# Kernel tuning notes

Measured on AMD Instinct MI355X. Metric: run time of the kernel, lower is better.

## Reference

```python
import jax, jax.numpy as jnp
import numpy as np
import math

B, S, D, H, FF, L = 8, 1024, 1024, 8, 4096, 2
DK = D // H
NEG = -1e32
EPS = 1e-5


def _cosine_pe(seq_len, d_model):
    pos = jnp.arange(seq_len, dtype=jnp.float32)[:, None]
    div = jnp.exp(jnp.arange(0, d_model, 2, dtype=jnp.float32) * (-(math.log(10000.0) / d_model)))
    pe = jnp.zeros((seq_len, d_model), dtype=jnp.float32)
    pe = pe.at[:, 0::2].set(jnp.sin(pos * div))
    pe = pe.at[:, 1::2].set(jnp.cos(pos * div))
    return pe


def setup_inputs() -> dict:
    key = jax.random.key(0)
    ks = jax.random.split(key, 12)
    sc = 0.02
    g = lambda k, shape: (jax.random.normal(k, shape, jnp.float32) * sc)
    return {
        "q_embed": jax.random.normal(ks[0], (B, S, D), jnp.float32),
        "qa_embed": jax.random.normal(ks[1], (B, S, D), jnp.float32),
        "pos_emb": _cosine_pe(S, D),
        "Wk": g(ks[2], (L, D, D)), "bk": jnp.zeros((L, D), jnp.float32),
        "Wv": g(ks[3], (L, D, D)), "bv": jnp.zeros((L, D), jnp.float32),
        "Wo": g(ks[4], (L, D, D)), "bo": jnp.zeros((L, D), jnp.float32),
        "ln1_g": jnp.ones((L, D), jnp.float32), "ln1_b": jnp.zeros((L, D), jnp.float32),
        "W1": g(ks[5], (L, FF, D)), "b1": jnp.zeros((L, FF), jnp.float32),
        "W2": g(ks[6], (L, D, FF)), "b2": jnp.zeros((L, D), jnp.float32),
        "ln2_g": jnp.ones((L, D), jnp.float32), "ln2_b": jnp.zeros((L, D), jnp.float32),
    }


def _layernorm(x, g, b):
    m = jnp.mean(x, axis=-1, keepdims=True)
    v = jnp.mean(jnp.square(x - m), axis=-1, keepdims=True)
    return (x - m) * jax.lax.rsqrt(v + EPS) * g + b


def _mha(x, y, Wk, bk, Wv, bv, Wo, bo, allow):
    # kq_same=1: q and k both come from k_linear applied to x (query==key input)
    k = (jnp.einsum('bsd,od->bso', x, Wk) + bk).reshape(B, S, H, DK).transpose(0, 2, 1, 3)
    q = k  # identical projection and identical input
    v = (jnp.einsum('bsd,od->bso', y, Wv) + bv).reshape(B, S, H, DK).transpose(0, 2, 1, 3)
    scores = jnp.einsum('bhqd,bhkd->bhqk', q, k) / math.sqrt(DK)
    scores = jnp.where(allow, scores, NEG)  # masked_fill(mask==0, -1e32)
    attn = jax.nn.softmax(scores, axis=-1)
    attn = attn.at[:, :, 0, :].set(0.0)  # zero_pad: first query row zeroed
    out = jnp.einsum('bhqk,bhkd->bhqd', attn, v)
    out = out.transpose(0, 2, 1, 3).reshape(B, S, D)
    return jnp.einsum('bsd,od->bso', out, Wo) + bo


def reference(q_embed, qa_embed, pos_emb, Wk, bk, Wv, bv, Wo, bo,
              ln1_g, ln1_b, W1, b1, W2, b2, ln2_g, ln2_b):
    x = q_embed + pos_emb[None]
    y = qa_embed + pos_emb[None]
    # strictly-lower-triangular allowed positions (triu(k=0)==0)
    allow = jnp.tril(jnp.ones((S, S), dtype=bool), -1)[None, None]
    for l in range(L):
        q2 = _mha(x, x, y, Wk[l], bk[l], Wv[l], bv[l], Wo[l], bo[l], allow) if False else _mha(x, y, Wk[l], bk[l], Wv[l], bv[l], Wo[l], bo[l], allow)
        x = _layernorm(x + q2, ln1_g[l], ln1_b[l])
        ff = jnp.einsum('bsf,df->bsd', jax.nn.relu(jnp.einsum('bsd,fd->bsf', x, W1[l]) + b1[l]), W2[l]) + b2[l]
        x = _layernorm(x + ff, ln2_g[l], ln2_b[l])
    return x
```

## Files before the change

kernel.cpp:

```cpp
#include <hip/hip_runtime.h>
#include <hip/hip_bf16.h>
#include <cstdint>
#include <cstddef>

#define B_  8
#define S_  1024
#define D_  1024
#define H_  8
#define FF_ 4096
#define L_  2
#define DK_ 128

typedef __bf16 bf16x8 __attribute__((ext_vector_type(8)));
typedef float  f32x4  __attribute__((ext_vector_type(4)));

__device__ __forceinline__ unsigned short f2bf(float f) {
    union { float f; uint32_t u; } v; v.f = f;
    uint32_t r = v.u + 0x7fffu + ((v.u >> 16) & 1u);
    return (unsigned short)(r >> 16);
}
__device__ __forceinline__ float bf2f(unsigned short u) {
    union { uint32_t u; float f; } v; v.u = ((uint32_t)u) << 16; return v.f;
}

__global__ __launch_bounds__(256) void init_xy(
    const float* __restrict__ qe, const float* __restrict__ qa,
    const float* __restrict__ pe,
    unsigned short* __restrict__ xb, unsigned short* __restrict__ yb)
{
    int i = (blockIdx.x * 256 + threadIdx.x) * 4;
    int pi = i & (S_ * D_ - 1);
    float4 q = *(const float4*)(qe + i);
    float4 a = *(const float4*)(qa + i);
    float4 p = *(const float4*)(pe + pi);
    ushort4 xo; xo.x = f2bf(q.x + p.x); xo.y = f2bf(q.y + p.y);
    xo.z = f2bf(q.z + p.z); xo.w = f2bf(q.w + p.w);
    ushort4 yo; yo.x = f2bf(a.x + p.x); yo.y = f2bf(a.y + p.y);
    yo.z = f2bf(a.z + p.z); yo.w = f2bf(a.w + p.w);
    *(ushort4*)(xb + i) = xo;
    *(ushort4*)(yb + i) = yo;
}

__global__ __launch_bounds__(256) void cvt_bf16(
    const float* __restrict__ in, unsigned short* __restrict__ out)
{
    int i = (blockIdx.x * 256 + threadIdx.x) * 4;
    float4 f = *(const float4*)(in + i);
    ushort4 o; o.x = f2bf(f.x); o.y = f2bf(f.y); o.z = f2bf(f.z); o.w = f2bf(f.w);
    *(ushort4*)(out + i) = o;
}

template<bool RELU, int OMODE>
__global__ __launch_bounds__(256) void gemm_bt(
    const unsigned short* __restrict__ A, const unsigned short* __restrict__ W,
    const float* __restrict__ bias, void* __restrict__ Cout,
    int M, int N, int K)
{
    __shared__ unsigned short sA[2][128][64];
    __shared__ unsigned short sW[2][128][64];

    const int tid  = threadIdx.x;
    const int lane = tid & 63;
    const int w    = tid >> 6;
    const int l16  = lane & 15;
    const int quad = lane >> 4;
    const int m0 = blockIdx.y * 128;
    const int n0 = blockIdx.x * 128;
    const int rw = (w >> 1) * 64;
    const int cw = (w & 1) * 64;

    const int srow   = lane >> 3;
    const int schunk = lane & 7;

    auto stage = [&](int k0, int buf) {
        #pragma unroll
        for (int i = 0; i < 4; ++i) {
            int r0  = w * 32 + i * 8;
            int row = r0 + srow;
            int gc  = schunk ^ (row & 7);
            const unsigned short* ga = A + (size_t)(m0 + row) * K + k0 + gc * 8;
            const unsigned short* gw = W + (size_t)(n0 + row) * K + k0 + gc * 8;
            __builtin_amdgcn_global_load_lds(
                (const __attribute__((address_space(1))) unsigned int*)ga,
                (__attribute__((address_space(3))) unsigned int*)&sA[buf][r0][0], 16, 0, 0);
            __builtin_amdgcn_global_load_lds(
                (const __attribute__((address_space(1))) unsigned int*)gw,
                (__attribute__((address_space(3))) unsigned int*)&sW[buf][r0][0], 16, 0, 0);
        }
    };

    f32x4 acc[4][4] = {};
    const int NK = K >> 6;
    int cur = 0;
    stage(0, 0);

    for (int kt = 0; kt < NK; ++kt) {
        __syncthreads();
        if (kt + 1 < NK) stage((kt + 1) << 6, cur ^ 1);

        #pragma unroll
        for (int ks = 0; ks < 2; ++ks) {
            bf16x8 af[4], wf[4];
            #pragma unroll
            for (int t = 0; t < 4; ++t) {
                int arow = rw + t * 16 + l16;
                int achk = (ks * 4 + quad) ^ (arow & 7);
                af[t] = *(const bf16x8*)&sA[cur][arow][achk * 8];
                int wrow = cw + t * 16 + l16;
                int wchk = (ks * 4 + quad) ^ (wrow & 7);
                wf[t] = *(const bf16x8*)&sW[cur][wrow][wchk * 8];
            }
            #pragma unroll
            for (int it = 0; it < 4; ++it)
                #pragma unroll
                for (int jt = 0; jt < 4; ++jt)
                    acc[it][jt] = __builtin_amdgcn_mfma_f32_16x16x32_bf16(
                        af[it], wf[jt], acc[it][jt], 0, 0, 0);
        }
        cur ^= 1;
    }

    #pragma unroll
    for (int it = 0; it < 4; ++it)
        #pragma unroll
        for (int jt = 0; jt < 4; ++jt) {
            int row = m0 + rw + it * 16 + quad * 4;
            int col = n0 + cw + jt * 16 + l16;
            float bcol = bias[col];
            float v[4];
            #pragma unroll
            for (int r = 0; r < 4; ++r) {
                v[r] = acc[it][jt][r] + bcol;
                if (RELU) v[r] = fmaxf(v[r], 0.0f);
            }
            if (OMODE == 1) {
                #pragma unroll
                for (int r = 0; r < 4; ++r)
                    ((unsigned short*)Cout)[(size_t)(row + r) * N + col] = f2bf(v[r]);
            } else {
                int key = row & (S_ - 1);
                int bb  = row >> 10;
                int hh  = col >> 7, dim = col & (DK_ - 1);
                unsigned short* dst = (unsigned short*)Cout
                    + ((size_t)(bb * H_ + hh) * DK_ + dim) * S_ + key;
                ushort4 o4; o4.x = f2bf(v[0]); o4.y = f2bf(v[1]);
                o4.z = f2bf(v[2]); o4.w = f2bf(v[3]);
                *(ushort4*)dst = o4;
            }
        }
}

template<bool RELU>
__global__ __launch_bounds__(512, 2) void gemm_bt8(
    const unsigned short* __restrict__ A, const unsigned short* __restrict__ W,
    const float* __restrict__ bias, unsigned short* __restrict__ Cout,
    int M, int N, int K)
{
    __shared__ unsigned short sA[2][256][64];
    __shared__ unsigned short sB[2][256][64];

    const int tid  = threadIdx.x;
    const int lane = tid & 63;
    const int w    = tid >> 6;
    const int l16  = lane & 15;
    const int quad = lane >> 4;
    const int wr   = w >> 2;
    const int wc   = w & 3;

    const int nwg = gridDim.x * gridDim.y;
    const int bid = blockIdx.y * gridDim.x + blockIdx.x;
    const int sb  = (bid & 7) * (nwg >> 3) + (bid >> 3);
    const int m0  = (sb / gridDim.x) * 256;
    const int n0  = (sb % gridDim.x) * 256;

    const int srow8 = lane >> 3;
    const int schk  = (lane & 7) ^ srow8;

    auto stA = [&](int i, int buf, int k0) {
        int r0 = i * 64 + w * 8;
        const unsigned short* g = A + (size_t)(m0 + r0 + srow8) * K + k0 + schk * 8;
        __builtin_amdgcn_global_load_lds(
            (const __attribute__((address_space(1))) unsigned int*)g,
            (__attribute__((address_space(3))) unsigned int*)&sA[buf][r0][0], 16, 0, 0);
    };
    auto stB = [&](int i, int buf, int k0) {
        int r0 = i * 64 + w * 8;
        const unsigned short* g = W + (size_t)(n0 + r0 + srow8) * K + k0 + schk * 8;
        __builtin_amdgcn_global_load_lds(
            (const __attribute__((address_space(1))) unsigned int*)g,
            (__attribute__((address_space(3))) unsigned int*)&sB[buf][r0][0], 16, 0, 0);
    };
    auto rdA = [&](int buf, int t, int ks) {
        int row = wr * 128 + t * 16 + l16;
        int chk = (ks * 4 + quad) ^ (row & 7);
        return *(const bf16x8*)&sA[buf][row][chk * 8];
    };
    auto rdB = [&](int buf, int j, int ks) {
        int row = wc * 64 + j * 16 + l16;
        int chk = (ks * 4 + quad) ^ (row & 7);
        return *(const bf16x8*)&sB[buf][row][chk * 8];
    };

    f32x4 acc[8][4] = {};
    const int NK = K >> 6;
    int cur = 0;

    stB(0, 0, 0); stB(1, 0, 0); stB(2, 0, 0); stB(3, 0, 0);
    stA(0, 0, 0); stA(2, 0, 0); stA(1, 0, 0); stA(3, 0, 0);
    asm volatile("s_waitcnt vmcnt(2)\n\ts_barrier" ::: "memory");

    for (int kt = 0; kt < NK; ++kt) {
        const bool pref = (kt + 1 < NK);
        const int  k1   = (kt + 1) << 6;
        const int  nb   = cur ^ 1;
        bf16x8 bfr[2][4];
        bf16x8 a0, a1, a2, a3;

        #pragma unroll
        for (int ks = 0; ks < 2; ++ks)
            #pragma unroll
            for (int j = 0; j < 4; ++j) bfr[ks][j] = rdB(cur, j, ks);
        a0 = rdA(cur, 0, 0); a1 = rdA(cur, 0, 1);
        a2 = rdA(cur, 1, 0); a3 = rdA(cur, 1, 1);
        if (pref) { stB(0, nb, k1); stB(1, nb, k1); stB(2, nb, k1); }
        __builtin_amdgcn_s_setprio(1);
        #pragma unroll
        for (int j = 0; j < 4; ++j) {
            acc[0][j] = __builtin_amdgcn_mfma_f32_16x16x32_bf16(a0, bfr[0][j], acc[0][j], 0, 0, 0);
            acc[1][j] = __builtin_amdgcn_mfma_f32_16x16x32_bf16(a2, bfr[0][j], acc[1][j], 0, 0, 0);
        }
        #pragma unroll
        for (int j = 0; j < 4; ++j) {
            acc[0][j] = __builtin_amdgcn_mfma_f32_16x16x32_bf16(a1, bfr[1][j], acc[0][j], 0, 0, 0);
            acc[1][j] = __builtin_amdgcn_mfma_f32_16x16x32_bf16(a3, bfr[1][j], acc[1][j], 0, 0, 0);
        }
        __builtin_amdgcn_s_setprio(0);
        asm volatile("s_barrier" ::: "memory");

        a0 = rdA(cur, 2, 0); a1 = rdA(cur, 2, 1);
        a2 = rdA(cur, 3, 0); a3 = rdA(cur, 3, 1);
        if (pref) { stB(3, nb, k1); stA(0, nb, k1); stA(2, nb, k1); }
        __builtin_amdgcn_s_setprio(1);
        #pragma unroll
        for (int j = 0; j < 4; ++j) {
            acc[2][j] = __builtin_amdgcn_mfma_f32_16x16x32_bf16(a0, bfr[0][j], acc[2][j], 0, 0, 0);
            acc[3][j] = __builtin_amdgcn_mfma_f32_16x16x32_bf16(a2, bfr[0][j], acc[3][j], 0, 0, 0);
        }
        #pragma unroll
        for (int j = 0; j < 4; ++j) {
            acc[2][j] = __builtin_amdgcn_mfma_f32_16x16x32_bf16(a1, bfr[1][j], acc[2][j], 0, 0, 0);
            acc[3][j] = __builtin_amdgcn_mfma_f32_16x16x32_bf16(a3, bfr[1][j], acc[3][j], 0, 0, 0);
        }
        __builtin_amdgcn_s_setprio(0);
        if (pref) asm volatile("s_waitcnt vmcnt(6)\n\ts_barrier" ::: "memory");
        else      asm volatile("s_waitcnt vmcnt(0)\n\ts_barrier" ::: "memory");

        a0 = rdA(cur, 4, 0); a1 = rdA(cur, 4, 1);
        a2 = rdA(cur, 5, 0); a3 = rdA(cur, 5, 1);
        if (pref) { stA(1, nb, k1); stA(3, nb, k1); }
        __builtin_amdgcn_s_setprio(1);
        #pragma unroll
        for (int j = 0; j < 4; ++j) {
            acc[4][j] = __builtin_amdgcn_mfma_f32_16x16x32_bf16(a0, bfr[0][j], acc[4][j], 0, 0, 0);
            acc[5][j] = __builtin_amdgcn_mfma_f32_16x16x32_bf16(a2, bfr[0][j], acc[5][j], 0, 0, 0);
        }
        #pragma unroll
        for (int j = 0; j < 4; ++j) {
            acc[4][j] = __builtin_amdgcn_mfma_f32_16x16x32_bf16(a1, bfr[1][j], acc[4][j], 0, 0, 0);
            acc[5][j] = __builtin_amdgcn_mfma_f32_16x16x32_bf16(a3, bfr[1][j], acc[5][j], 0, 0, 0);
        }
        __builtin_amdgcn_s_setprio(0);
        asm volatile("s_barrier" ::: "memory");

        a0 = rdA(cur, 6, 0); a1 = rdA(cur, 6, 1);
        a2 = rdA(cur, 7, 0); a3 = rdA(cur, 7, 1);
        __builtin_amdgcn_s_setprio(1);
        #pragma unroll
        for (int j = 0; j < 4; ++j) {
            acc[6][j] = __builtin_amdgcn_mfma_f32_16x16x32_bf16(a0, bfr[0][j], acc[6][j], 0, 0, 0);
            acc[7][j] = __builtin_amdgcn_mfma_f32_16x16x32_bf16(a2, bfr[0][j], acc[7][j], 0, 0, 0);
        }
        #pragma unroll
        for (int j = 0; j < 4; ++j) {
            acc[6][j] = __builtin_amdgcn_mfma_f32_16x16x32_bf16(a1, bfr[1][j], acc[6][j], 0, 0, 0);
            acc[7][j] = __builtin_amdgcn_mfma_f32_16x16x32_bf16(a3, bfr[1][j], acc[7][j], 0, 0, 0);
        }
        __builtin_amdgcn_s_setprio(0);
        asm volatile("s_waitcnt vmcnt(2)\n\ts_barrier" ::: "memory");
        cur = nb;
    }

    #pragma unroll
    for (int t = 0; t < 8; ++t)
        #pragma unroll
        for (int j = 0; j < 4; ++j) {
            int row = m0 + wr * 128 + t * 16 + quad * 4;
            int col = n0 + wc * 64 + j * 16 + l16;
            float bcol = bias[col];
            #pragma unroll
            for (int r = 0; r < 4; ++r) {
                float v = acc[t][j][r] + bcol;
                if (RELU) v = fmaxf(v, 0.0f);
                Cout[(size_t)(row + r) * N + col] = f2bf(v);
            }
        }
}

__global__ __launch_bounds__(512, 2) void gemm_sk(
    const unsigned short* __restrict__ A, const unsigned short* __restrict__ W,
    float* __restrict__ P, int M, int N, int K, int Kh)
{
    __shared__ unsigned short sA[2][256][64];
    __shared__ unsigned short sB[2][256][64];

    const int tid  = threadIdx.x;
    const int lane = tid & 63;
    const int w    = tid >> 6;
    const int l16  = lane & 15;
    const int quad = lane >> 4;
    const int wr   = w >> 2;
    const int wc   = w & 3;

    const int nwg = gridDim.x * gridDim.y;
    const int bid = blockIdx.y * gridDim.x + blockIdx.x;
    const int sb  = (bid & 7) * (nwg >> 3) + (bid >> 3);
    const int m0  = (sb / gridDim.x) * 256;
    const int n0  = (sb % gridDim.x) * 256;
    const int kb  = blockIdx.z * Kh;
    P += (size_t)blockIdx.z * M * N;

    const int srow8 = lane >> 3;
    const int schk  = (lane & 7) ^ srow8;

    auto stA = [&](int i, int buf, int k0) {
        int r0 = i * 64 + w * 8;
        const unsigned short* g = A + (size_t)(m0 + r0 + srow8) * K + k0 + schk * 8;
        __builtin_amdgcn_global_load_lds(
            (const __attribute__((address_space(1))) unsigned int*)g,
            (__attribute__((address_space(3))) unsigned int*)&sA[buf][r0][0], 16, 0, 0);
    };
    auto stB = [&](int i, int buf, int k0) {
        int r0 = i * 64 + w * 8;
        const unsigned short* g = W + (size_t)(n0 + r0 + srow8) * K + k0 + schk * 8;
        __builtin_amdgcn_global_load_lds(
            (const __attribute__((address_space(1))) unsigned int*)g,
            (__attribute__((address_space(3))) unsigned int*)&sB[buf][r0][0], 16, 0, 0);
    };
    auto rdA = [&](int buf, int t, int ks) {
        int row = wr * 128 + t * 16 + l16;
        int chk = (ks * 4 + quad) ^ (row & 7);
        return *(const bf16x8*)&sA[buf][row][chk * 8];
    };
    auto rdB = [&](int buf, int j, int ks) {
        int row = wc * 64 + j * 16 + l16;
        int chk = (ks * 4 + quad) ^ (row & 7);
        return *(const bf16x8*)&sB[buf][row][chk * 8];
    };

    f32x4 acc[8][4] = {};
    const int NK = Kh >> 6;
    int cur = 0;

    stB(0, 0, kb); stB(1, 0, kb); stB(2, 0, kb); stB(3, 0, kb);
    stA(0, 0, kb); stA(2, 0, kb); stA(1, 0, kb); stA(3, 0, kb);
    asm volatile("s_waitcnt vmcnt(2)\n\ts_barrier" ::: "memory");

    for (int kt = 0; kt < NK; ++kt) {
        const bool pref = (kt + 1 < NK);
        const int  k1   = kb + ((kt + 1) << 6);
        const int  nb   = cur ^ 1;
        bf16x8 bfr[2][4];
        bf16x8 a0, a1, a2, a3;

        #pragma unroll
        for (int ks = 0; ks < 2; ++ks)
            #pragma unroll
            for (int j = 0; j < 4; ++j) bfr[ks][j] = rdB(cur, j, ks);
        a0 = rdA(cur, 0, 0); a1 = rdA(cur, 0, 1);
        a2 = rdA(cur, 1, 0); a3 = rdA(cur, 1, 1);
        if (pref) { stB(0, nb, k1); stB(1, nb, k1); stB(2, nb, k1); }
        __builtin_amdgcn_s_setprio(1);
        #pragma unroll
        for (int j = 0; j < 4; ++j) {
            acc[0][j] = __builtin_amdgcn_mfma_f32_16x16x32_bf16(a0, bfr[0][j], acc[0][j], 0, 0, 0);
            acc[1][j] = __builtin_amdgcn_mfma_f32_16x16x32_bf16(a2, bfr[0][j], acc[1][j], 0, 0, 0);
        }
        #pragma unroll
        for (int j = 0; j < 4; ++j) {
            acc[0][j] = __builtin_amdgcn_mfma_f32_16x16x32_bf16(a1, bfr[1][j], acc[0][j], 0, 0, 0);
            acc[1][j] = __builtin_amdgcn_mfma_f32_16x16x32_bf16(a3, bfr[1][j], acc[1][j], 0, 0, 0);
        }
        __builtin_amdgcn_s_setprio(0);
        asm volatile("s_barrier" ::: "memory");

        a0 = rdA(cur, 2, 0); a1 = rdA(cur, 2, 1);
        a2 = rdA(cur, 3, 0); a3 = rdA(cur, 3, 1);
        if (pref) { stB(3, nb, k1); stA(0, nb, k1); stA(2, nb, k1); }
        __builtin_amdgcn_s_setprio(1);
        #pragma unroll
        for (int j = 0; j < 4; ++j) {
            acc[2][j] = __builtin_amdgcn_mfma_f32_16x16x32_bf16(a0, bfr[0][j], acc[2][j], 0, 0, 0);
            acc[3][j] = __builtin_amdgcn_mfma_f32_16x16x32_bf16(a2, bfr[0][j], acc[3][j], 0, 0, 0);
        }
        #pragma unroll
        for (int j = 0; j < 4; ++j) {
            acc[2][j] = __builtin_amdgcn_mfma_f32_16x16x32_bf16(a1, bfr[1][j], acc[2][j], 0, 0, 0);
            acc[3][j] = __builtin_amdgcn_mfma_f32_16x16x32_bf16(a3, bfr[1][j], acc[3][j], 0, 0, 0);
        }
        __builtin_amdgcn_s_setprio(0);
        if (pref) asm volatile("s_waitcnt vmcnt(6)\n\ts_barrier" ::: "memory");
        else      asm volatile("s_waitcnt vmcnt(0)\n\ts_barrier" ::: "memory");

        a0 = rdA(cur, 4, 0); a1 = rdA(cur, 4, 1);
        a2 = rdA(cur, 5, 0); a3 = rdA(cur, 5, 1);
        if (pref) { stA(1, nb, k1); stA(3, nb, k1); }
        __builtin_amdgcn_s_setprio(1);
        #pragma unroll
        for (int j = 0; j < 4; ++j) {
            acc[4][j] = __builtin_amdgcn_mfma_f32_16x16x32_bf16(a0, bfr[0][j], acc[4][j], 0, 0, 0);
            acc[5][j] = __builtin_amdgcn_mfma_f32_16x16x32_bf16(a2, bfr[0][j], acc[5][j], 0, 0, 0);
        }
        #pragma unroll
        for (int j = 0; j < 4; ++j) {
            acc[4][j] = __builtin_amdgcn_mfma_f32_16x16x32_bf16(a1, bfr[1][j], acc[4][j], 0, 0, 0);
            acc[5][j] = __builtin_amdgcn_mfma_f32_16x16x32_bf16(a3, bfr[1][j], acc[5][j], 0, 0, 0);
        }
        __builtin_amdgcn_s_setprio(0);
        asm volatile("s_barrier" ::: "memory");

        a0 = rdA(cur, 6, 0); a1 = rdA(cur, 6, 1);
        a2 = rdA(cur, 7, 0); a3 = rdA(cur, 7, 1);
        __builtin_amdgcn_s_setprio(1);
        #pragma unroll
        for (int j = 0; j < 4; ++j) {
            acc[6][j] = __builtin_amdgcn_mfma_f32_16x16x32_bf16(a0, bfr[0][j], acc[6][j], 0, 0, 0);
            acc[7][j] = __builtin_amdgcn_mfma_f32_16x16x32_bf16(a2, bfr[0][j], acc[7][j], 0, 0, 0);
        }
        #pragma unroll
        for (int j = 0; j < 4; ++j) {
            acc[6][j] = __builtin_amdgcn_mfma_f32_16x16x32_bf16(a1, bfr[1][j], acc[6][j], 0, 0, 0);
            acc[7][j] = __builtin_amdgcn_mfma_f32_16x16x32_bf16(a3, bfr[1][j], acc[7][j], 0, 0, 0);
        }
        __builtin_amdgcn_s_setprio(0);
        asm volatile("s_waitcnt vmcnt(2)\n\ts_barrier" ::: "memory");
        cur = nb;
    }

    #pragma unroll
    for (int t = 0; t < 8; ++t)
        #pragma unroll
        for (int j = 0; j < 4; ++j) {
            int row = m0 + wr * 128 + t * 16 + quad * 4;
            int col = n0 + wc * 64 + j * 16 + l16;
            #pragma unroll
            for (int r = 0; r < 4; ++r)
                P[(size_t)(row + r) * N + col] = acc[t][j][r];
        }
}

__global__ __launch_bounds__(256) void attn_mfma(
    const unsigned short* __restrict__ Kbuf, const unsigned short* __restrict__ Vtbuf,
    unsigned short* __restrict__ Obuf)
{
    __shared__ unsigned short sK[2][64][128];
    __shared__ unsigned short sVt[2][128][64];
    __shared__ unsigned short sP[4][16][72];

    const int tid  = threadIdx.x;
    const int lane = tid & 63;
    const int w    = tid >> 6;
    const int l16  = lane & 15;
    const int quad = lane >> 4;

    const int ib   = blockIdx.y * 8 + blockIdx.x;
    const int pa   = (ib >> 3) & 7;
    const int bh   = (ib & 7) + ((ib >> 6) << 3);
    const int b    = bh >> 3, h = bh & 7;
    const unsigned short* KB  = Kbuf  + ((size_t)b * S_) * D_ + h * DK_;
    const unsigned short* VTB = Vtbuf + (size_t)bh * DK_ * S_;

    const float scale = 0.08838834764831845f;

    auto stageK = [&](int kt, int buf) {
        #pragma unroll
        for (int i = 0; i < 4; ++i) {
            int r0  = w * 16 + i * 4;
            int row = r0 + (lane >> 4);
            int c   = (lane & 15) ^ (row & 15);
            const unsigned short* g = KB + (size_t)(kt * 64 + row) * D_ + c * 8;
            __builtin_amdgcn_global_load_lds(
                (const __attribute__((address_space(1))) unsigned int*)g,
                (__attribute__((address_space(3))) unsigned int*)&sK[buf][r0][0], 16, 0, 0);
        }
    };
    auto stageV = [&](int kt, int buf) {
        #pragma unroll
        for (int i = 0; i < 4; ++i) {
            int r0  = w * 32 + i * 8;
            int row = r0 + (lane >> 3);
            int c   = (lane & 7) ^ (row & 7);
            const unsigned short* g = VTB + (size_t)row * S_ + kt * 64 + c * 8;
            __builtin_amdgcn_global_load_lds(
                (const __attribute__((address_space(1))) unsigned int*)g,
                (__attribute__((address_space(3))) unsigned int*)&sVt[buf][r0][0], 16, 0, 0);
        }
    };

    #pragma unroll
    for (int half = 0; half < 2; ++half) {
        const int qt = half == 0 ? (15 - pa) : pa;
        const int q0 = qt * 64;

        bf16x8 qf[4];
        {
            const unsigned short* qrow = KB + (size_t)(q0 + w * 16 + l16) * D_ + quad * 8;
            #pragma unroll
            for (int ks = 0; ks < 4; ++ks)
                qf[ks] = *(const bf16x8*)(qrow + ks * 32);
        }
        asm volatile("s_waitcnt vmcnt(0)\n\ts_barrier" ::: "memory");

        f32x4 Oacc[8] = {};
        float m_run[4] = {-1e30f, -1e30f, -1e30f, -1e30f};
        float l_run[4] = {};

        int cur = 0;
        stageK(0, 0); stageV(0, 0);

        for (int kt = 0; kt <= qt; ++kt) {
            const int nb = cur ^ 1;
            asm volatile("s_waitcnt vmcnt(4)\n\ts_barrier" ::: "memory");
            if (kt < qt) stageK(kt + 1, nb);

            f32x4 sacc[4];
            __builtin_amdgcn_s_setprio(1);
            #pragma unroll
            for (int nt = 0; nt < 4; ++nt) {
                f32x4 a = {};
                #pragma unroll
                for (int ks = 0; ks < 4; ++ks) {
                    int kr = nt * 16 + l16;
                    int p  = (ks * 4 + quad) ^ (kr & 15);
                    bf16x8 kf = *(const bf16x8*)&sK[cur][kr][p * 8];
                    a = __builtin_amdgcn_mfma_f32_16x16x32_bf16(qf[ks], kf, a, 0, 0, 0);
                }
                sacc[nt] = a;
            }
            __builtin_amdgcn_s_setprio(0);

            const bool diag = (kt == qt);
            #pragma unroll
            for (int nt = 0; nt < 4; ++nt)
                #pragma unroll
                for (int r = 0; r < 4; ++r) {
                    float v = sacc[nt][r] * scale;
                    if (diag) {
                        int nidx = nt * 16 + l16;
                        int midx = w * 16 + quad * 4 + r;
                        if (nidx >= midx) v = -1e30f;
                    }
                    sacc[nt][r] = v;
                }

            float mx[4];
            #pragma unroll
            for (int r = 0; r < 4; ++r) {
                float m = fmaxf(fmaxf(sacc[0][r], sacc[1][r]), fmaxf(sacc[2][r], sacc[3][r]));
                m = fmaxf(m, __shfl_xor(m, 1));
                m = fmaxf(m, __shfl_xor(m, 2));
                m = fmaxf(m, __shfl_xor(m, 4));
                m = fmaxf(m, __shfl_xor(m, 8));
                mx[r] = m;
            }
            bool need = false;
            #pragma unroll
            for (int r = 0; r < 4; ++r) need |= (mx[r] > m_run[r] + 8.0f);
            if (__any(need)) {
                #pragma unroll
                for (int r = 0; r < 4; ++r) {
                    float mn = fmaxf(m_run[r], mx[r]);
                    float alpha = __expf(m_run[r] - mn);
                    m_run[r] = mn;
                    l_run[r] *= alpha;
                    #pragma unroll
                    for (int o = 0; o < 8; ++o) Oacc[o][r] *= alpha;
                }
            }
            #pragma unroll
            for (int r = 0; r < 4; ++r) {
                float rs = 0.0f;
                #pragma unroll
                for (int nt = 0; nt < 4; ++nt) {
                    float e = __expf(sacc[nt][r] - m_run[r]);
                    sacc[nt][r] = e;
                    rs += e;
                }
                rs += __shfl_xor(rs, 1);
                rs += __shfl_xor(rs, 2);
                rs += __shfl_xor(rs, 4);
                rs += __shfl_xor(rs, 8);
                l_run[r] += rs;
            }

            if (kt < qt) stageV(kt + 1, nb);

            #pragma unroll
            for (int nt = 0; nt < 4; ++nt)
                #pragma unroll
                for (int r = 0; r < 4; ++r)
                    sP[w][quad * 4 + r][nt * 16 + l16] = f2bf(sacc[nt][r]);

            bf16x8 pf[2];
            #pragma unroll
            for (int ks = 0; ks < 2; ++ks)
                pf[ks] = *(const bf16x8*)&sP[w][l16][ks * 32 + quad * 8];

            if (kt < qt) asm volatile("s_waitcnt vmcnt(8)\n\ts_barrier" ::: "memory");
            else         asm volatile("s_waitcnt vmcnt(0)\n\ts_barrier" ::: "memory");

            __builtin_amdgcn_s_setprio(1);
            #pragma unroll
            for (int nt = 0; nt < 8; ++nt) {
                #pragma unroll
                for (int ks = 0; ks < 2; ++ks) {
                    int vr = nt * 16 + l16;
                    int p  = (ks * 4 + quad) ^ (vr & 7);
                    bf16x8 vf = *(const bf16x8*)&sVt[cur][vr][p * 8];
                    Oacc[nt] = __builtin_amdgcn_mfma_f32_16x16x32_bf16(pf[ks], vf, Oacc[nt], 0, 0, 0);
                }
            }
            __builtin_amdgcn_s_setprio(0);
            cur = nb;
        }

        float inv[4];
        #pragma unroll
        for (int r = 0; r < 4; ++r) {
            int m = q0 + w * 16 + quad * 4 + r;
            inv[r] = (l_run[r] > 0.0f && m != 0) ? 1.0f / l_run[r] : 0.0f;
        }
        #pragma unroll
        for (int nt = 0; nt < 8; ++nt)
            #pragma unroll
            for (int r = 0; r < 4; ++r) {
                int m = q0 + w * 16 + quad * 4 + r;
                Obuf[((size_t)b * S_ + m) * D_ + h * DK_ + nt * 16 + l16] =
                    f2bf(Oacc[nt][r] * inv[r]);
            }
    }
}

template<bool FINAL>
__global__ __launch_bounds__(256) void ln_res(
    const unsigned short* __restrict__ xin, const unsigned short* __restrict__ delta,
    const float* __restrict__ g, const float* __restrict__ bta,
    unsigned short* __restrict__ xbout, float* __restrict__ fout)
{
    __shared__ float red1[4], red2[4];
    const int row = blockIdx.x;
    const int tid = threadIdx.x;
    const int c = tid * 4;
    ushort4 xu = *(const ushort4*)(xin + (size_t)row * D_ + c);
    ushort4 du = *(const ushort4*)(delta + (size_t)row * D_ + c);
    float t0 = bf2f(xu.x) + bf2f(du.x), t1 = bf2f(xu.y) + bf2f(du.y);
    float t2 = bf2f(xu.z) + bf2f(du.z), t3 = bf2f(xu.w) + bf2f(du.w);

    float s = t0 + t1 + t2 + t3;
    #pragma unroll
    for (int off = 32; off > 0; off >>= 1) s += __shfl_down(s, off);
    if ((tid & 63) == 0) red1[tid >> 6] = s;
    __syncthreads();
    float mean = (red1[0] + red1[1] + red1[2] + red1[3]) * (1.0f / 1024.0f);

    float e0 = t0 - mean, e1 = t1 - mean, e2 = t2 - mean, e3 = t3 - mean;
    float ss = e0 * e0 + e1 * e1 + e2 * e2 + e3 * e3;
    #pragma unroll
    for (int off = 32; off > 0; off >>= 1) ss += __shfl_down(ss, off);
    if ((tid & 63) == 0) red2[tid >> 6] = ss;
    __syncthreads();
    float var = (red2[0] + red2[1] + red2[2] + red2[3]) * (1.0f / 1024.0f);
    float rstd = rsqrtf(var + 1e-5f);

    float4 gv = *(const float4*)(g + c);
    float4 bv = *(const float4*)(bta + c);
    float o0 = e0 * rstd * gv.x + bv.x;
    float o1 = e1 * rstd * gv.y + bv.y;
    float o2 = e2 * rstd * gv.z + bv.z;
    float o3 = e3 * rstd * gv.w + bv.w;
    if (FINAL) {
        *(float4*)(fout + (size_t)row * D_ + c) = make_float4(o0, o1, o2, o3);
    } else {
        ushort4 ob; ob.x = f2bf(o0); ob.y = f2bf(o1); ob.z = f2bf(o2); ob.w = f2bf(o3);
        *(ushort4*)(xbout + (size_t)row * D_ + c) = ob;
    }
}

template<bool FINAL>
__global__ __launch_bounds__(256) void ln_res_sk(
    const unsigned short* __restrict__ xin,
    const float* __restrict__ p0, const float* __restrict__ p1,
    const float* __restrict__ wbias,
    const float* __restrict__ g, const float* __restrict__ bta,
    unsigned short* __restrict__ xbout, float* __restrict__ fout)
{
    __shared__ float red1[4], red2[4];
    const int row = blockIdx.x;
    const int tid = threadIdx.x;
    const int c = tid * 4;
    ushort4 xu = *(const ushort4*)(xin + (size_t)row * D_ + c);
    float4 a0 = *(const float4*)(p0 + (size_t)row * D_ + c);
    float4 a1 = *(const float4*)(p1 + (size_t)row * D_ + c);
    float4 wb = *(const float4*)(wbias + c);
    float t0 = bf2f(xu.x) + a0.x + a1.x + wb.x;
    float t1 = bf2f(xu.y) + a0.y + a1.y + wb.y;
    float t2 = bf2f(xu.z) + a0.z + a1.z + wb.z;
    float t3 = bf2f(xu.w) + a0.w + a1.w + wb.w;

    float s = t0 + t1 + t2 + t3;
    #pragma unroll
    for (int off = 32; off > 0; off >>= 1) s += __shfl_down(s, off);
    if ((tid & 63) == 0) red1[tid >> 6] = s;
    __syncthreads();
    float mean = (red1[0] + red1[1] + red1[2] + red1[3]) * (1.0f / 1024.0f);

    float e0 = t0 - mean, e1 = t1 - mean, e2 = t2 - mean, e3 = t3 - mean;
    float ss = e0 * e0 + e1 * e1 + e2 * e2 + e3 * e3;
    #pragma unroll
    for (int off = 32; off > 0; off >>= 1) ss += __shfl_down(ss, off);
    if ((tid & 63) == 0) red2[tid >> 6] = ss;
    __syncthreads();
    float var = (red2[0] + red2[1] + red2[2] + red2[3]) * (1.0f / 1024.0f);
    float rstd = rsqrtf(var + 1e-5f);

    float4 gv = *(const float4*)(g + c);
    float4 bv = *(const float4*)(bta + c);
    float o0 = e0 * rstd * gv.x + bv.x;
    float o1 = e1 * rstd * gv.y + bv.y;
    float o2 = e2 * rstd * gv.z + bv.z;
    float o3 = e3 * rstd * gv.w + bv.w;
    if (FINAL) {
        *(float4*)(fout + (size_t)row * D_ + c) = make_float4(o0, o1, o2, o3);
    } else {
        ushort4 ob; ob.x = f2bf(o0); ob.y = f2bf(o1); ob.z = f2bf(o2); ob.w = f2bf(o3);
        *(ushort4*)(xbout + (size_t)row * D_ + c) = ob;
    }
}

extern "C" void kernel_launch(void* const* d_in, const int* in_sizes, int n_in,
                              void* d_out, int out_size, void* d_ws, size_t ws_size,
                              hipStream_t stream)
{
    const float* qe   = (const float*)d_in[0];
    const float* qa   = (const float*)d_in[1];
    const float* pe   = (const float*)d_in[2];
    const float* Wk   = (const float*)d_in[3];
    const float* bk   = (const float*)d_in[4];
    const float* Wv   = (const float*)d_in[5];
    const float* bv   = (const float*)d_in[6];
    const float* Wo   = (const float*)d_in[7];
    const float* bo   = (const float*)d_in[8];
    const float* ln1g = (const float*)d_in[9];
    const float* ln1b = (const float*)d_in[10];
    const float* W1   = (const float*)d_in[11];
    const float* b1   = (const float*)d_in[12];
    const float* W2   = (const float*)d_in[13];
    const float* b2   = (const float*)d_in[14];
    const float* ln2g = (const float*)d_in[15];
    const float* ln2b = (const float*)d_in[16];

    const size_t BSD = (size_t)B_ * S_ * D_;
    const size_t BSF = (size_t)B_ * S_ * FF_;
    const size_t WDD = (size_t)D_ * D_;
    const size_t WFD = (size_t)FF_ * D_;

    char* p = (char*)d_ws;
    auto take = [&](size_t bytes) { char* r = p; p += (bytes + 255) & ~255ULL; return r; };
    unsigned short* xb    = (unsigned short*)take(BSD * 2);
    unsigned short* yb    = (unsigned short*)take(BSD * 2);
    unsigned short* delta = (unsigned short*)take(BSD * 2);
    char*           uni   = take(BSF * 2);
    unsigned short* Kb    = (unsigned short*)uni;
    unsigned short* Vt    = Kb + BSD;
    unsigned short* attnb = Vt + BSD;
    unsigned short* hb    = (unsigned short*)uni;
    unsigned short* wslot = (unsigned short*)take(WFD * 2);

    const size_t base_used = (size_t)(p - (char*)d_ws);
    const bool   use_sk    = ws_size >= base_used + BSD * 8 + 256;
    float* pbuf = use_sk ? (float*)take(BSD * 8) : nullptr;

    init_xy<<<(int)(BSD / 4 / 256), 256, 0, stream>>>(qe, qa, pe, xb, yb);

    const int M = B_ * S_;
    for (int l = 0; l < L_; ++l) {
        cvt_bf16<<<(int)(WDD / 1024), 256, 0, stream>>>(Wk + l * WDD, wslot);
        gemm_bt<false, 1><<<dim3(D_ / 128, M / 128), 256, 0, stream>>>(
            xb, wslot, bk + l * D_, Kb, M, D_, D_);
        cvt_bf16<<<(int)(WDD / 1024), 256, 0, stream>>>(Wv + l * WDD, wslot);
        gemm_bt<false, 2><<<dim3(D_ / 128, M / 128), 256, 0, stream>>>(
            yb, wslot, bv + l * D_, Vt, M, D_, D_);
        attn_mfma<<<dim3(8, B_ * H_), 256, 0, stream>>>(Kb, Vt, attnb);
        cvt_bf16<<<(int)(WDD / 1024), 256, 0, stream>>>(Wo + l * WDD, wslot);
        gemm_bt<false, 1><<<dim3(D_ / 128, M / 128), 256, 0, stream>>>(
            attnb, wslot, bo + l * D_, delta, M, D_, D_);
        ln_res<false><<<M, 256, 0, stream>>>(xb, delta, ln1g + l * D_, ln1b + l * D_, xb, nullptr);
        cvt_bf16<<<(int)(WFD / 1024), 256, 0, stream>>>(W1 + l * WFD, wslot);
        gemm_bt8<true><<<dim3(FF_ / 256, M / 256), 512, 0, stream>>>(
            xb, wslot, b1 + l * FF_, hb, M, FF_, D_);
        cvt_bf16<<<(int)(WFD / 1024), 256, 0, stream>>>(W2 + l * WFD, wslot);
        if (use_sk) {
            gemm_sk<<<dim3(D_ / 256, M / 256, 2), 512, 0, stream>>>(
                hb, wslot, pbuf, M, D_, FF_, FF_ / 2);
            if (l == L_ - 1)
                ln_res_sk<true><<<M, 256, 0, stream>>>(
                    xb, pbuf, pbuf + BSD, b2 + l * D_,
                    ln2g + l * D_, ln2b + l * D_, nullptr, (float*)d_out);
            else
                ln_res_sk<false><<<M, 256, 0, stream>>>(
                    xb, pbuf, pbuf + BSD, b2 + l * D_,
                    ln2g + l * D_, ln2b + l * D_, xb, nullptr);
        } else {
            gemm_bt<false, 1><<<dim3(D_ / 128, M / 128), 256, 0, stream>>>(
                hb, wslot, b2 + l * D_, delta, M, D_, FF_);
            if (l == L_ - 1)
                ln_res<true><<<M, 256, 0, stream>>>(xb, delta, ln2g + l * D_, ln2b + l * D_,
                                                   nullptr, (float*)d_out);
            else
                ln_res<false><<<M, 256, 0, stream>>>(xb, delta, ln2g + l * D_, ln2b + l * D_,
                                                    xb, nullptr);
        }
    }
}
```

Measured before the change: 790.2 us.

## Load V fragments directly from global into registers, drop V LDS staging

The attention kernel no longer stages V^T tiles through shared memory. Each wave loads its V fragments straight from global into registers at the start of every key tile, and the launch bounds now request 3 blocks per CU. The aim is to cut LDS footprint and the extra barrier so occupancy rises, at the cost of redundant global loads across waves, higher register pressure (16 bf16x8 per lane), and V latency that is hidden only by the QK and softmax work. The explicit vmcnt-based waits are replaced by a plain __syncthreads, which may also change how overlapped K prefetches behave.

```diff
diff --git a/kernel.cpp b/kernel.cpp
--- a/kernel.cpp
+++ b/kernel.cpp
@@ -458,12 +458,11 @@
         }
 }
 
-__global__ __launch_bounds__(256) void attn_mfma(
+__global__ __launch_bounds__(256, 3) void attn_mfma(
     const unsigned short* __restrict__ Kbuf, const unsigned short* __restrict__ Vtbuf,
     unsigned short* __restrict__ Obuf)
 {
     __shared__ unsigned short sK[2][64][128];
-    __shared__ unsigned short sVt[2][128][64];
     __shared__ unsigned short sP[4][16][72];
 
     const int tid  = threadIdx.x;
@@ -493,18 +492,6 @@
                 (__attribute__((address_space(3))) unsigned int*)&sK[buf][r0][0], 16, 0, 0);
         }
     };
-    auto stageV = [&](int kt, int buf) {
-        #pragma unroll
-        for (int i = 0; i < 4; ++i) {
-            int r0  = w * 32 + i * 8;
-            int row = r0 + (lane >> 3);
-            int c   = (lane & 7) ^ (row & 7);
-            const unsigned short* g = VTB + (size_t)row * S_ + kt * 64 + c * 8;
-            __builtin_amdgcn_global_load_lds(
-                (const __attribute__((address_space(1))) unsigned int*)g,
-                (__attribute__((address_space(3))) unsigned int*)&sVt[buf][r0][0], 16, 0, 0);
-        }
-    };
 
     #pragma unroll
     for (int half = 0; half < 2; ++half) {
@@ -525,11 +512,22 @@
         float l_run[4] = {};
 
         int cur = 0;
-        stageK(0, 0); stageV(0, 0);
+        stageK(0, 0);
 
         for (int kt = 0; kt <= qt; ++kt) {
             const int nb = cur ^ 1;
-            asm volatile("s_waitcnt vmcnt(4)\n\ts_barrier" ::: "memory");
+            __syncthreads();
+
+            bf16x8 vfr[8][2];
+            #pragma unroll
+            for (int nt = 0; nt < 8; ++nt)
+                #pragma unroll
+                for (int ks = 0; ks < 2; ++ks) {
+                    int vr = nt * 16 + l16;
+                    vfr[nt][ks] = *(const bf16x8*)(
+                        VTB + (size_t)vr * S_ + kt * 64 + (ks * 4 + quad) * 8);
+                }
+
             if (kt < qt) stageK(kt + 1, nb);
 
             f32x4 sacc[4];
@@ -602,8 +600,6 @@
                 l_run[r] += rs;
             }
 
-            if (kt < qt) stageV(kt + 1, nb);
-
             #pragma unroll
             for (int nt = 0; nt < 4; ++nt)
                 #pragma unroll
@@ -615,19 +611,13 @@
             for (int ks = 0; ks < 2; ++ks)
                 pf[ks] = *(const bf16x8*)&sP[w][l16][ks * 32 + quad * 8];
 
-            if (kt < qt) asm volatile("s_waitcnt vmcnt(8)\n\ts_barrier" ::: "memory");
-            else         asm volatile("s_waitcnt vmcnt(0)\n\ts_barrier" ::: "memory");
-
             __builtin_amdgcn_s_setprio(1);
             #pragma unroll
             for (int nt = 0; nt < 8; ++nt) {
                 #pragma unroll
-                for (int ks = 0; ks < 2; ++ks) {
-                    int vr = nt * 16 + l16;
-                    int p  = (ks * 4 + quad) ^ (vr & 7);
-                    bf16x8 vf = *(const bf16x8*)&sVt[cur][vr][p * 8];
-                    Oacc[nt] = __builtin_amdgcn_mfma_f32_16x16x32_bf16(pf[ks], vf, Oacc[nt], 0, 0, 0);
-                }
+                for (int ks = 0; ks < 2; ++ks)
+                    Oacc[nt] = __builtin_amdgcn_mfma_f32_16x16x32_bf16(
+                        pf[ks], vfr[nt][ks], Oacc[nt], 0, 0, 0);
             }
             __builtin_amdgcn_s_setprio(0);
             cur = nb;
```

Measured after the change: 880.2 us. +11.4%, slower.
